# Kernel optimization log

Measured on AMD Instinct MI355X. Metric: run time of the kernel, lower is better.

Reference implementation:

```python
import jax, jax.numpy as jnp
import numpy as np

LW = (1.0, 1.0, 1.0)          # loss_weight
TLW = (0.1, 1.0)              # Total_loss_weight
TRIPLET_W = np.array([1.17236407, 1.0166286, 1.19620973, 0.5544405, 0.63531401, 0.51258428,
                      1.08866652, 1.15795989, 1.07389395, 0.98728399, 1.12754142, 1.05953744,
                      1.16945323, 1.15512349, 1.02097204, 1.15795989, 1.07147279, 0.50627649,
                      1.07147279, 0.61697221, 1.16367678, 1.0231585, 1.18416106, 1.04329092,
                      1.10645159, 1.18416106, 1.15795989, 1.16367678, 0.73949534, 0.78760821,
                      1.08617476, 1.00805777], dtype=np.float32)


def _lsa(cost):
    """Hungarian algorithm (Jonker-Volgenant / e-maxx potentials), equivalent to
    scipy.optimize.linear_sum_assignment for rectangular matrices."""
    cost = np.asarray(cost, dtype=np.float64)
    T = cost.shape[0] > cost.shape[1]
    C = cost.T if T else cost
    n, m = C.shape
    u = np.zeros(n + 1); v = np.zeros(m + 1)
    p = np.zeros(m + 1, dtype=np.int64)
    way = np.zeros(m + 1, dtype=np.int64)
    for i in range(1, n + 1):
        p[0] = i; j0 = 0
        minv = np.full(m + 1, np.inf)
        used = np.zeros(m + 1, dtype=bool)
        while True:
            used[j0] = True
            i0 = p[j0]
            cur = C[i0 - 1] - u[i0] - v[1:]
            free = ~used[1:]
            upd = free & (cur < minv[1:])
            minv[1:] = np.where(upd, cur, minv[1:])
            way[1:] = np.where(upd, j0, way[1:])
            js = np.where(free)[0]
            j1 = js[np.argmin(minv[1:][js])] + 1
            delta = minv[j1]
            u[p[used]] += delta
            v[used] -= delta
            minv[~used] -= delta
            j0 = j1
            if p[j0] == 0:
                break
        while j0:
            j1 = way[j0]; p[j0] = p[j1]; j0 = j1
    cols = np.arange(m)
    sel = p[1:] > 0
    r, c = p[1:][sel] - 1, cols[sel]
    order = np.argsort(r)
    r, c = r[order], c[order]
    return (c, r) if T else (r, c)


def _cost_matrix(pred_head, pred_rel, pred_tail, iid, vid, tid):
    # per-element weighted CrossEntropyLoss over a single sample reduces to plain
    # -log_softmax at the target (the class weight cancels in the 'mean' reduction)
    def nll(logits, tgt, C):
        logp = jax.nn.log_softmax(logits, axis=-1)           # [B,Q,C]
        oh = jax.nn.one_hot(tgt, C, dtype=logp.dtype)        # [B,G,C]
        return -jnp.einsum('bqc,bgc->bqg', logp, oh)         # [B,Q,G]
    return (LW[0] * nll(pred_head, iid, 9)
            + LW[1] * nll(pred_rel, vid, 13)
            + LW[2] * nll(pred_tail, tid, 2))


def setup_inputs() -> dict:
    key = jax.random.key(0)
    ks = jax.random.split(key, 12)
    B, Q, G = 256, 300, 16
    return {
        'pred_head': jax.random.normal(ks[0], (B, Q, 9), jnp.float32),
        'pred_rel': jax.random.normal(ks[1], (B, Q, 13), jnp.float32),
        'pred_tail': jax.random.normal(ks[2], (B, Q, 2), jnp.float32),
        'IVT': jax.random.normal(ks[3], (B, 32), jnp.float32),
        'instrumentId': jax.random.randint(ks[4], (B, G), 0, 9, jnp.int32),
        'verbId': jax.random.randint(ks[5], (B, G), 0, 13, jnp.int32),
        'targetId': jax.random.randint(ks[6], (B, G), 0, 2, jnp.int32),
        'instrument': jax.random.randint(ks[7], (B, G), 0, 9, jnp.int32),
        'verb': jax.random.randint(ks[8], (B, G), 0, 13, jnp.int32),
        'target': jax.random.randint(ks[9], (B, G), 0, 2, jnp.int32),
        'triplet': jax.random.randint(ks[10], (B, 32), 0, 2, jnp.int32),
        'mask': jnp.ones((B, G), jnp.int32),
    }


def reference(pred_head, pred_rel, pred_tail, IVT, instrumentId, verbId, targetId,
              instrument, verb, target, triplet, mask):
    sim = _cost_matrix(pred_head, pred_rel, pred_tail, instrumentId, verbId, targetId)  # [B,Q,G]
    # masked_fill(inf) on invalid gt columns (no-op for all-ones mask, kept for fidelity)
    sim_filled = jnp.where((mask == 0)[:, None, :], jnp.inf, sim)
    sim_np = np.asarray(jax.device_get(sim_filled))
    mask_np = np.asarray(jax.device_get(mask))
    b_list, r_list, c_list = [], [], []
    for i in range(sim_np.shape[0]):
        nval = int(mask_np[i].sum())
        r, c = _lsa(sim_np[i][:, :nval])
        b_list.append(np.full(len(r), i, dtype=np.int64))
        r_list.append(r); c_list.append(c)
    b_idx = jnp.asarray(np.concatenate(b_list))
    r_idx = jnp.asarray(np.concatenate(r_list))
    c_idx = jnp.asarray(np.concatenate(c_list))
    loss1 = sim_filled[b_idx, r_idx, c_idx].mean()
    # weighted BCEWithLogitsLoss (weight scales per-element loss; mean over all elements)
    x = IVT
    t = triplet.astype(jnp.float32)
    bce = jnp.maximum(x, 0.0) - x * t + jnp.log1p(jnp.exp(-jnp.abs(x)))
    loss5 = (jnp.asarray(TRIPLET_W) * bce).mean()
    return TLW[0] * loss1 + TLW[1] * loss5
```

## Files before the change

### kernel.cpp

```cpp
#include <hip/hip_runtime.h>
#include <hip/hip_bf16.h>


#define BT 512
#define NW 8
#define NQ 300
#define NG 16
#define NT 5
#define SH 2700
#define SR 3900
#define ST 900

__device__ const float d_tw[32] = {
    1.17236407f, 1.0166286f,  1.19620973f, 0.5544405f,  0.63531401f, 0.51258428f,
    1.08866652f, 1.15795989f, 1.07389395f, 0.98728399f, 1.12754142f, 1.05953744f,
    1.16945323f, 1.15512349f, 1.02097204f, 1.15795989f, 1.07147279f, 0.50627649f,
    1.07147279f, 0.61697221f, 1.16367678f, 1.0231585f,  1.18416106f, 1.04329092f,
    1.10645159f, 1.18416106f, 1.15795989f, 1.16367678f, 0.73949534f, 0.78760821f,
    1.08617476f, 1.00805777f};

__device__ __forceinline__ float wave_min_bcast(float x) {
    int t;
    t = __builtin_amdgcn_update_dpp(__float_as_int(x), __float_as_int(x), 0x111, 0xF, 0xF, false);
    x = fminf(x, __int_as_float(t));
    t = __builtin_amdgcn_update_dpp(__float_as_int(x), __float_as_int(x), 0x112, 0xF, 0xF, false);
    x = fminf(x, __int_as_float(t));
    t = __builtin_amdgcn_update_dpp(__float_as_int(x), __float_as_int(x), 0x114, 0xF, 0xF, false);
    x = fminf(x, __int_as_float(t));
    t = __builtin_amdgcn_update_dpp(__float_as_int(x), __float_as_int(x), 0x118, 0xF, 0xF, false);
    x = fminf(x, __int_as_float(t));
    t = __builtin_amdgcn_update_dpp(__float_as_int(x), __float_as_int(x), 0x142, 0xF, 0xF, false);
    x = fminf(x, __int_as_float(t));
    t = __builtin_amdgcn_update_dpp(__float_as_int(x), __float_as_int(x), 0x143, 0xF, 0xF, false);
    x = fminf(x, __int_as_float(t));
    return __int_as_float(__builtin_amdgcn_readlane(__float_as_int(x), 63));
}

__global__ __launch_bounds__(BT) void SetCriterion_14482629722575_kernel(
    const float* __restrict__ ph, const float* __restrict__ pr,
    const float* __restrict__ pt, const float* __restrict__ ivt,
    const int* __restrict__ iid, const int* __restrict__ vid,
    const int* __restrict__ tid_, const int* __restrict__ trip,
    float* __restrict__ out)
{
    const int b    = blockIdx.x;
    const int tid  = threadIdx.x;
    const int wave = tid >> 6;
    const int lane = tid & 63;
    const float FINF = 3.0e38f;

    __shared__ __align__(16) float stage[SH + SR + ST];
    __shared__ float cost[NG * NQ];
    __shared__ float pmin[NW][NG];
    __shared__ int   pjm[NW][NG];
    __shared__ int   sgi[NG], sgv[NG], sgt[NG];

    float* sh_ = stage;
    float* sr_ = stage + SH;
    float* st_ = stage + SH + SR;

    {
        const float4* s4 = (const float4*)(ph + (size_t)b * SH);
        float4* d4 = (float4*)sh_;
        for (int i = tid; i < SH / 4; i += BT) d4[i] = s4[i];
    }
    {
        const float4* s4 = (const float4*)(pr + (size_t)b * SR);
        float4* d4 = (float4*)sr_;
        for (int i = tid; i < SR / 4; i += BT) d4[i] = s4[i];
    }
    {
        const float2* s2 = (const float2*)(pt + (size_t)b * (NQ * 2));
        for (int i = tid; i < NQ; i += BT) {
            const float2 v = s2[i];
            st_[i * 3]     = v.x;
            st_[i * 3 + 1] = v.y;
        }
    }
    if (tid < NG) {
        sgi[tid] = iid[b * NG + tid];
        sgv[tid] = vid[b * NG + tid];
        sgt[tid] = tid_[b * NG + tid];
    }
    __syncthreads();

    int gi[NG], gv[NG], gc[NG];
    #pragma unroll
    for (int i = 0; i < NG; i++) { gi[i] = sgi[i]; gv[i] = sgv[i]; gc[i] = sgt[i]; }

    float rmin[NG]; int rjm[NG];
    #pragma unroll
    for (int i = 0; i < NG; i++) { rmin[i] = FINF; rjm[i] = 0; }

    if (tid < NQ) {
        const int q = tid;
        float lh, lr, lt;
        {
            const float* x = sh_ + q * 9;
            float r[9];
            #pragma unroll
            for (int c = 0; c < 9; c++) r[c] = x[c];
            float m = r[0];
            #pragma unroll
            for (int c = 1; c < 9; c++) m = fmaxf(m, r[c]);
            float sE = 0.f;
            #pragma unroll
            for (int c = 0; c < 9; c++) sE += __expf(r[c] - m);
            lh = m + __logf(sE);
        }
        {
            const float* x = sr_ + q * 13;
            float r[13];
            #pragma unroll
            for (int c = 0; c < 13; c++) r[c] = x[c];
            float m = r[0];
            #pragma unroll
            for (int c = 1; c < 13; c++) m = fmaxf(m, r[c]);
            float sE = 0.f;
            #pragma unroll
            for (int c = 0; c < 13; c++) sE += __expf(r[c] - m);
            lr = m + __logf(sE);
        }
        {
            const float r0 = st_[q * 3], r1 = st_[q * 3 + 1];
            const float m = fmaxf(r0, r1);
            lt = m + __logf(__expf(r0 - m) + __expf(r1 - m));
        }
        const float lsum = lh + lr + lt;
        #pragma unroll
        for (int i = 0; i < NG; i++) {
            const float c = lsum -
                (sh_[q * 9 + gi[i]] + sr_[q * 13 + gv[i]] + st_[q * 3 + gc[i]]);
            cost[i * NQ + q] = c;
            rmin[i] = c; rjm[i] = q + 1;
        }
    }

    #pragma unroll
    for (int i = 0; i < NG; i++) {
        const float m = wave_min_bcast(rmin[i]);
        const unsigned long long msk = __ballot(rmin[i] == m);
        const int l0 = (int)__ffsll(msk) - 1;
        const int jm = __builtin_amdgcn_readlane(rjm[i], l0);
        if (lane == 0) { pmin[wave][i] = m; pjm[wave][i] = jm; }
    }
    __syncthreads();

    if (wave == 1) {
        float bs = 0.f;
        if (lane < 32) {
            const float x  = ivt[b * 32 + lane];
            const float tt = (float)trip[b * 32 + lane];
            const float e  = __expf(-fabsf(x));
            bs = d_tw[lane] * (fmaxf(x, 0.f) - x * tt + __logf(1.f + e));
        }
        #pragma unroll
        for (int off = 32; off >= 1; off >>= 1) bs += __shfl_xor(bs, off);
        if (lane == 0) atomicAdd(out, bs / 8192.0f);
        return;
    }
    if (wave != 0) return;

    float um[NG]; int jm_[NG];
    #pragma unroll
    for (int i = 0; i < NG; i++) {
        float m = pmin[0][i]; int jm = pjm[0][i];
        #pragma unroll
        for (int w = 1; w < NW; w++) {
            const float mw = pmin[w][i]; const int jw = pjm[w][i];
            if (mw < m) { m = mw; jm = jw; }
        }
        um[i] = m; jm_[i] = jm;
    }

    float v_[NT], minv_[NT];
    int   way_[NT], par_[NT];
    bool  valid[NT];
    #pragma unroll
    for (int t = 0; t < NT; t++) {
        valid[t] = (t * 64 + lane + 1 <= NQ);
        v_[t] = 0.f; par_[t] = 0; way_[t] = 0; minv_[t] = FINF;
    }

    int pending = 0;
    #pragma unroll
    for (int i = 1; i < NG; i++) {
        bool conf = false;
        #pragma unroll
        for (int k = 0; k < NG; k++)
            if (k < i && jm_[k] == jm_[i]) conf = true;
        if (conf) pending |= 1 << i;
    }
    #pragma unroll
    for (int i = 0; i < NG; i++) {
        if (!((pending >> i) & 1)) {
            const int jm = jm_[i];
            const int slot = (jm - 1) >> 6, owner = (jm - 1) & 63;
            #pragma unroll
            for (int t = 0; t < NT; t++)
                if (slot == t && lane == owner) par_[t] = i + 1;
        }
    }

    while (pending) {
        const int r = __ffs(pending);
        pending &= pending - 1;
        #pragma unroll
        for (int t = 0; t < NT; t++) minv_[t] = FINF;
        unsigned usedbits = 0;
        float u0 = 0.f;
        #pragma unroll
        for (int i = 0; i < NG; i++) if (r == i + 1) u0 = um[i];
        int i0 = r, j0 = 0, guard = 0;

        while (true) {
            if (j0 && ((j0 - 1) & 63) == lane) usedbits |= 1u << ((j0 - 1) >> 6);

            const int rowbase = (i0 - 1) * NQ;
            float raw[NT];
            #pragma unroll
            for (int t = 0; t < NT; t++) {
                const int j = t * 64 + lane + 1;
                raw[t] = (valid[t] ? cost[rowbase + j - 1] : FINF) - v_[t];
            }

            float lmin = FINF;
            int   lmeta = 0x7FFFFFFF;
            #pragma unroll
            for (int t = 0; t < NT; t++) {
                if (valid[t] && !((usedbits >> t) & 1u)) {
                    const float cur = raw[t] - u0;
                    if (cur < minv_[t]) { minv_[t] = cur; way_[t] = j0; }
                    if (minv_[t] < lmin) {
                        lmin = minv_[t];
                        lmeta = ((t * 64 + lane + 1) << 5) | par_[t];
                    }
                }
            }
            const float delta = wave_min_bcast(lmin);
            const unsigned long long msk = __ballot(lmin == delta);
            const int l0 = (int)__ffsll(msk) - 1;
            const int meta = __builtin_amdgcn_readlane(lmeta, l0);
            const int j1 = meta >> 5, i1 = meta & 31;

            #pragma unroll
            for (int t = 0; t < NT; t++) {
                if ((usedbits >> t) & 1u) v_[t] -= delta;
                else                      minv_[t] -= delta;
            }

            if (i1 == 0) { j0 = j1; break; }

            {
                const int slot = (j1 - 1) >> 6, owner = (j1 - 1) & 63;
                float vsel = v_[0];
                #pragma unroll
                for (int t = 1; t < NT; t++) if (slot == t) vsel = v_[t];
                const float vj1 = __int_as_float(
                    __builtin_amdgcn_readlane(__float_as_int(vsel), owner));
                u0 = cost[(i1 - 1) * NQ + (j1 - 1)] - vj1;
            }
            j0 = j1; i0 = i1;
            if (++guard > 40) break;
        }

        int jj = j0;
        while (jj) {
            const int slot = (jj - 1) >> 6, owner = (jj - 1) & 63;
            int wsel = way_[0];
            #pragma unroll
            for (int t = 1; t < NT; t++) if (slot == t) wsel = way_[t];
            const int wj = __builtin_amdgcn_readlane(wsel, owner);
            int pj;
            if (wj == 0) pj = r;
            else {
                const int s2 = (wj - 1) >> 6, o2 = (wj - 1) & 63;
                int psel = par_[0];
                #pragma unroll
                for (int t = 1; t < NT; t++) if (s2 == t) psel = par_[t];
                pj = __builtin_amdgcn_readlane(psel, o2);
            }
            #pragma unroll
            for (int t = 0; t < NT; t++)
                if (slot == t && ((jj - 1) & 63) == lane) par_[t] = pj;
            jj = wj;
        }
    }

    float s = 0.f;
    #pragma unroll
    for (int t = 0; t < NT; t++) {
        const int j = t * 64 + lane + 1;
        if (valid[t] && par_[t] > 0)
            s += cost[(par_[t] - 1) * NQ + (j - 1)];
    }
    #pragma unroll
    for (int off = 32; off >= 1; off >>= 1) s += __shfl_xor(s, off);

    if (lane == 0)
        atomicAdd(out, 0.1f * (s / 4096.0f));
}

extern "C" void kernel_launch(void* const* d_in, const int* in_sizes, int n_in,
                              void* d_out, int out_size, void* d_ws, size_t ws_size,
                              hipStream_t stream) {
    (void)in_sizes; (void)n_in; (void)d_ws; (void)ws_size; (void)out_size;

    const float* pred_head    = (const float*)d_in[0];
    const float* pred_rel     = (const float*)d_in[1];
    const float* pred_tail    = (const float*)d_in[2];
    const float* IVT          = (const float*)d_in[3];
    const int*   instrumentId = (const int*)d_in[4];
    const int*   verbId       = (const int*)d_in[5];
    const int*   targetId     = (const int*)d_in[6];
    const int*   triplet      = (const int*)d_in[10];

    hipMemsetAsync(d_out, 0, 4, stream);

    SetCriterion_14482629722575_kernel<<<256, BT, 0, stream>>>(
        pred_head, pred_rel, pred_tail, IVT,
        instrumentId, verbId, targetId, triplet, (float*)d_out);
}
```

Before: 94.41 us.

## Partition input staging per wave to drop block barrier and shrink block

Each wave now copies into shared memory only the head, relation and tail logit rows for its own 64 queries. The block-wide barrier after staging is replaced by a per-wave LDS wait, and the block shrinks from 8 waves to 5, which exactly covers the 300 queries. Ground-truth ids and BCE inputs are loaded straight into registers at kernel start instead of going through shared memory, hiding their latency behind the staging. The cost is hard-coded per-wave offsets that depend on the row sizes and the query count, and the serial assignment phase in wave 0 is left unchanged.

Result: faster. 91.93 us (-2.6%).

```diff
diff --git a/kernel.cpp b/kernel.cpp
--- a/kernel.cpp
+++ b/kernel.cpp
@@ -1,9 +1,8 @@
 #include <hip/hip_runtime.h>
-#include <hip/hip_bf16.h>
-
-
-#define BT 512
-#define NW 8
+
+
+#define BT 320
+#define NW 5
 #define NQ 300
 #define NG 16
 #define NT 5
@@ -53,40 +52,51 @@
     __shared__ float cost[NG * NQ];
     __shared__ float pmin[NW][NG];
     __shared__ int   pjm[NW][NG];
-    __shared__ int   sgi[NG], sgv[NG], sgt[NG];
 
     float* sh_ = stage;
     float* sr_ = stage + SH;
     float* st_ = stage + SH + SR;
 
+    float bce_x = 0.f, bce_t = 0.f;
+    if (wave == 1 && lane < 32) {
+        bce_x = ivt[b * 32 + lane];
+        bce_t = (float)trip[b * 32 + lane];
+    }
+
+    int gi[NG], gv[NG], gc[NG];
+    #pragma unroll
+    for (int i = 0; i < NG; i++) {
+        gi[i] = iid[b * NG + i];
+        gv[i] = vid[b * NG + i];
+        gc[i] = tid_[b * NG + i];
+    }
+
     {
         const float4* s4 = (const float4*)(ph + (size_t)b * SH);
         float4* d4 = (float4*)sh_;
-        for (int i = tid; i < SH / 4; i += BT) d4[i] = s4[i];
+        const int hi = (144 * (wave + 1) < SH / 4) ? 144 * (wave + 1) : SH / 4;
+        for (int k = 144 * wave + lane; k < hi; k += 64) d4[k] = s4[k];
     }
     {
         const float4* s4 = (const float4*)(pr + (size_t)b * SR);
         float4* d4 = (float4*)sr_;
-        for (int i = tid; i < SR / 4; i += BT) d4[i] = s4[i];
+        const int hi = (208 * (wave + 1) < SR / 4) ? 208 * (wave + 1) : SR / 4;
+        for (int k = 208 * wave + lane; k < hi; k += 64) d4[k] = s4[k];
     }
     {
-        const float2* s2 = (const float2*)(pt + (size_t)b * (NQ * 2));
-        for (int i = tid; i < NQ; i += BT) {
-            const float2 v = s2[i];
-            st_[i * 3]     = v.x;
-            st_[i * 3 + 1] = v.y;
-        }
-    }
-    if (tid < NG) {
-        sgi[tid] = iid[b * NG + tid];
-        sgv[tid] = vid[b * NG + tid];
-        sgt[tid] = tid_[b * NG + tid];
-    }
-    __syncthreads();
-
-    int gi[NG], gv[NG], gc[NG];
-    #pragma unroll
-    for (int i = 0; i < NG; i++) { gi[i] = sgi[i]; gv[i] = sgv[i]; gc[i] = sgt[i]; }
+        const float4* s4 = (const float4*)(pt + (size_t)b * (NQ * 2));
+        const int hi = (32 * (wave + 1) < 150) ? 32 * (wave + 1) : 150;
+        const int k = 32 * wave + lane;
+        if (lane < 32 && k < hi) {
+            const float4 v = s4[k];
+            const int r0 = 2 * k, r1 = 2 * k + 1;
+            st_[r0 * 3]     = v.x;
+            st_[r0 * 3 + 1] = v.y;
+            st_[r1 * 3]     = v.z;
+            st_[r1 * 3 + 1] = v.w;
+        }
+    }
+    asm volatile("s_waitcnt lgkmcnt(0)" ::: "memory");
 
     float rmin[NG]; int rjm[NG];
     #pragma unroll
@@ -149,10 +159,9 @@
     if (wave == 1) {
         float bs = 0.f;
         if (lane < 32) {
-            const float x  = ivt[b * 32 + lane];
-            const float tt = (float)trip[b * 32 + lane];
-            const float e  = __expf(-fabsf(x));
-            bs = d_tw[lane] * (fmaxf(x, 0.f) - x * tt + __logf(1.f + e));
+            const float x = bce_x;
+            const float e = __expf(-fabsf(x));
+            bs = d_tw[lane] * (fmaxf(x, 0.f) - x * bce_t + __logf(1.f + e));
         }
         #pragma unroll
         for (int off = 32; off >= 1; off >>= 1) bs += __shfl_xor(bs, off);
```
